# Performance work log

Measured on AMD Instinct MI355X. Metric: run time of the kernel, lower is better.

## Reference

```python
import jax, jax.numpy as jnp
import numpy as np

H = 128
NH = 8
HD = H // NH  # 16
TANH_ALPHA = 10.0
LN_EPS = 1e-5


def _layer_norm(x, g, b):
    mu = jnp.mean(x, axis=-1, keepdims=True)
    var = jnp.mean((x - mu) ** 2, axis=-1, keepdims=True)
    return (x - mu) / jnp.sqrt(var + LN_EPS) * g + b


def setup_inputs() -> dict:
    key = jax.random.key(0)
    ks = jax.random.split(key, 24)
    B, N = 1024, 500

    def p(k, shape):
        return jax.random.normal(k, shape, dtype=jnp.float32) * 0.05

    inp = {
        "node_embeddings": jax.random.normal(ks[0], (B, N, H), jnp.float32),
        "graph_embeddings": jax.random.normal(ks[1], (B, H), jnp.float32),
        "first_node": jax.random.randint(ks[2], (B,), 0, N, jnp.int32),
        "current_node": jax.random.randint(ks[3], (B,), 0, N, jnp.int32),
        "mask": jax.random.randint(ks[4], (B, N), 0, 2, jnp.int32),
        # linear_first: Linear(384, 128)
        "W_first": p(ks[5], (H, 3 * H)),
        "b_first": p(ks[6], (H,)),
        # ln1 / ln2
        "g1": jnp.ones((H,), jnp.float32),
        "beta1": jnp.zeros((H,), jnp.float32),
        "g2": jnp.ones((H,), jnp.float32),
        "beta2": jnp.zeros((H,), jnp.float32),
        # LSTM(128,128) single layer, gate order i,f,g,o
        "W_ih": p(ks[7], (4 * H, H)),
        "W_hh": p(ks[8], (4 * H, H)),
        "b_ih": p(ks[9], (4 * H,)),
        "b_hh": p(ks[10], (4 * H,)),
        # attention / output projections (no bias)
        "Wq": p(ks[11], (H, H)),
        "Wk": p(ks[12], (H, H)),
        "Wv": p(ks[13], (H, H)),
        "Wproj": p(ks[14], (H, H)),
        # logitk: Linear(128,128) with bias
        "Wlk": p(ks[15], (H, H)),
        "blk": p(ks[16], (H,)),
    }
    return inp


def reference(node_embeddings, graph_embeddings, W_first, b_first, g1, beta1,
              W_ih, W_hh, b_ih, b_hh, g2, beta2, Wq, Wk, Wv, Wproj, Wlk, blk,
              first_node, current_node, mask):
    B, N, _ = node_embeddings.shape
    dt = node_embeddings.dtype

    # build_cache: K/V/logitK projections of all node embeddings
    ck = node_embeddings @ Wk.T                # [B,N,128]
    cv = node_embeddings @ Wv.T                # [B,N,128]
    lk = node_embeddings @ Wlk.T + blk         # [B,N,128]

    # context construction
    bidx = jnp.arange(B)
    first_emb = node_embeddings[bidx, first_node]    # [B,128]
    cur_emb = node_embeddings[bidx, current_node]    # [B,128]
    context = jnp.concatenate([graph_embeddings, first_emb, cur_emb], axis=1)
    context = _layer_norm(context @ W_first.T + b_first, g1, beta1)

    # single LSTM step from zero state (build_cache resets h,c to 0)
    gates = context @ W_ih.T + b_ih + b_hh           # h_prev = 0 -> no W_hh term
    i, f, g, o = jnp.split(gates, 4, axis=-1)
    c = jax.nn.sigmoid(i) * jnp.tanh(g)              # c_prev = 0
    h = jax.nn.sigmoid(o) * jnp.tanh(c)
    ctx = _layer_norm(h, g2, beta2)

    # multi-head single-query attention; note (e h) split: head is the FAST dim
    q = (ctx @ Wq.T).reshape(B, HD, NH).transpose(0, 2, 1)       # [B,h,e]
    k = ck.reshape(B, N, HD, NH).transpose(0, 3, 1, 2)           # [B,h,N,e]
    v = cv.reshape(B, N, HD, NH).transpose(0, 3, 1, 2)           # [B,h,N,e]
    maskf = mask.astype(dt)
    scores = jnp.einsum('bhe,bhne->bhn', q, k) / np.sqrt(HD) + maskf[:, None, :]
    att = jax.nn.softmax(scores, axis=-1)
    oh = jnp.einsum('bhn,bhne->bhe', att, v)                     # [B,h,e]
    att_out = oh.reshape(B, H)                                   # (h e): h slow, e fast

    context_emb = att_out @ Wproj.T                              # [B,128]
    comp = jnp.einsum('be,bne->bn', lk, context_emb[:, None, :].squeeze(1)[:, :][None].squeeze(0) if False else context_emb) if False else jnp.einsum('bne,be->bn', lk, context_emb)
    comp = comp / np.sqrt(H)
    comp = TANH_ALPHA * jnp.tanh(comp)
    out = jnp.where(mask == 1, -jnp.inf, comp)
    return out
```

## Files before the change

kernel.cpp:

```cpp
#include <hip/hip_runtime.h>
#include <math.h>

#define NBATCH 1024
#define NNODE  500
#define HDIM   128
#define NHEAD  8
#define G1K    4
#define RSQRT_H 0.08838834764831845f
#define MASK_NEG (-1e30f)

__device__ __forceinline__ float wave_sum64(float v) {
    #pragma unroll
    for (int off = 32; off >= 1; off >>= 1) v += __shfl_xor(v, off, 64);
    return v;
}
__device__ __forceinline__ float wave_max64(float v) {
    #pragma unroll
    for (int off = 32; off >= 1; off >>= 1) v = fmaxf(v, __shfl_xor(v, off, 64));
    return v;
}

template<int G>
__device__ __forceinline__ void block_ln(float (&x)[G], const float* __restrict__ gw,
                                         const float* __restrict__ bw,
                                         int t, int lane, int wv, float (*wpart)[G])
{
    float s[G];
    #pragma unroll
    for (int g = 0; g < G; ++g) s[g] = x[g];
    #pragma unroll
    for (int off = 32; off >= 1; off >>= 1) {
        #pragma unroll
        for (int g = 0; g < G; ++g) s[g] += __shfl_xor(s[g], off, 64);
    }
    if (lane == 0) {
        #pragma unroll
        for (int g = 0; g < G; ++g) wpart[wv][g] = s[g];
    }
    __syncthreads();
    float mu[G];
    #pragma unroll
    for (int g = 0; g < G; ++g) mu[g] = (wpart[0][g] + wpart[1][g]) * (1.f/128.f);
    __syncthreads();
    #pragma unroll
    for (int g = 0; g < G; ++g) { float d = x[g] - mu[g]; s[g] = d * d; }
    #pragma unroll
    for (int off = 32; off >= 1; off >>= 1) {
        #pragma unroll
        for (int g = 0; g < G; ++g) s[g] += __shfl_xor(s[g], off, 64);
    }
    if (lane == 0) {
        #pragma unroll
        for (int g = 0; g < G; ++g) wpart[wv][g] = s[g];
    }
    __syncthreads();
    float gv = gw[t], bv = bw[t];
    #pragma unroll
    for (int g = 0; g < G; ++g) {
        float var = (wpart[0][g] + wpart[1][g]) * (1.f/128.f);
        x[g] = (x[g] - mu[g]) / sqrtf(var + 1e-5f) * gv + bv;
    }
    __syncthreads();
}

__global__ __launch_bounds__(128) void k1_context(
    const float* __restrict__ node, const float* __restrict__ graph,
    const int* __restrict__ firstn, const int* __restrict__ curn,
    const float* __restrict__ W_first, const float* __restrict__ b_first,
    const float* __restrict__ g1, const float* __restrict__ beta1,
    const float* __restrict__ W_ih, const float* __restrict__ b_ih,
    const float* __restrict__ b_hh, const float* __restrict__ g2,
    const float* __restrict__ beta2, const float* __restrict__ Wq,
    const float* __restrict__ Wk, float* __restrict__ qW_out)
{
    const int t = threadIdx.x;
    const int lane = t & 63, wv = t >> 6;
    const int b0 = blockIdx.x * G1K;
    __shared__ float ctx[G1K][384];
    __shared__ float bufB[G1K][128];
    __shared__ float wpart[2][G1K];

    #pragma unroll
    for (int g = 0; g < G1K; ++g) {
        int b = b0 + g;
        ctx[g][t]       = graph[b*HDIM + t];
        ctx[g][128 + t] = node[((size_t)b*NNODE + firstn[b])*HDIM + t];
        ctx[g][256 + t] = node[((size_t)b*NNODE + curn[b])*HDIM + t];
    }
    __syncthreads();

    float x[G1K];
    {
        float bf = b_first[t];
        #pragma unroll
        for (int g = 0; g < G1K; ++g) x[g] = bf;
        for (int j = 0; j < 384; ++j) {
            float w = W_first[t*384 + j];
            #pragma unroll
            for (int g = 0; g < G1K; ++g) x[g] += ctx[g][j] * w;
        }
    }
    block_ln<G1K>(x, g1, beta1, t, lane, wv, wpart);

    #pragma unroll
    for (int g = 0; g < G1K; ++g) bufB[g][t] = x[g];
    __syncthreads();

    float gi[G1K], gg[G1K], go[G1K];
    {
        float bi = b_ih[t]       + b_hh[t];
        float bg = b_ih[256 + t] + b_hh[256 + t];
        float bo = b_ih[384 + t] + b_hh[384 + t];
        #pragma unroll
        for (int g = 0; g < G1K; ++g) { gi[g] = bi; gg[g] = bg; go[g] = bo; }
        for (int j = 0; j < 128; ++j) {
            float wi = W_ih[(size_t)t*128 + j];
            float wg = W_ih[(size_t)(256 + t)*128 + j];
            float wo = W_ih[(size_t)(384 + t)*128 + j];
            #pragma unroll
            for (int g = 0; g < G1K; ++g) {
                float v = bufB[g][j];
                gi[g] += v * wi; gg[g] += v * wg; go[g] += v * wo;
            }
        }
    }
    #pragma unroll
    for (int g = 0; g < G1K; ++g) {
        float ig = 1.f / (1.f + expf(-gi[g]));
        float cc = ig * tanhf(gg[g]);
        float og = 1.f / (1.f + expf(-go[g]));
        x[g] = og * tanhf(cc);
    }
    block_ln<G1K>(x, g2, beta2, t, lane, wv, wpart);

    #pragma unroll
    for (int g = 0; g < G1K; ++g) bufB[g][t] = x[g];
    __syncthreads();

    float q8[G1K];
    #pragma unroll
    for (int g = 0; g < G1K; ++g) q8[g] = 0.f;
    for (int j = 0; j < 128; ++j) {
        float w = Wq[t*128 + j];
        #pragma unroll
        for (int g = 0; g < G1K; ++g) q8[g] += bufB[g][j] * w;
    }
    __syncthreads();
    #pragma unroll
    for (int g = 0; g < G1K; ++g) bufB[g][t] = q8[g];
    __syncthreads();

    for (int h = 0; h < NHEAD; ++h) {
        float a[G1K];
        #pragma unroll
        for (int g = 0; g < G1K; ++g) a[g] = 0.f;
        for (int e = 0; e < 16; ++e) {
            float w = Wk[(e*8 + h)*HDIM + t];
            #pragma unroll
            for (int g = 0; g < G1K; ++g) a[g] += bufB[g][e*8 + h] * w;
        }
        #pragma unroll
        for (int g = 0; g < G1K; ++g)
            qW_out[((size_t)(b0 + g)*NHEAD + h)*HDIM + t] = 0.25f * a[g];
    }
}

__global__ __launch_bounds__(256) void k2_flash(
    const float* __restrict__ node, const int* __restrict__ mask,
    const float* __restrict__ qW, const float* __restrict__ Wv,
    const float* __restrict__ Wproj, const float* __restrict__ Wlk,
    const float* __restrict__ blk, float* __restrict__ wce_out,
    float* __restrict__ bias_out)
{
    const int b = blockIdx.x;
    const int tid = threadIdx.x;
    const int lane = tid & 63;
    const int wave = tid >> 6;

    __shared__ float4 s_tile[64*32];
    __shared__ __align__(16) float s_qw[NHEAD*HDIM];
    __shared__ float  s_p[NHEAD*64];
    __shared__ float  s_m[NHEAD], s_l[NHEAD], s_c[NHEAD];
    __shared__ float  s_ao[HDIM], s_ce[HDIM];

    ((float4*)s_qw)[tid] = ((const float4*)(qW + (size_t)b*NHEAD*HDIM))[tid];
    if (tid < NHEAD) { s_m[tid] = -INFINITY; s_l[tid] = 0.f; }

    float4 acc[NHEAD];
    #pragma unroll
    for (int h = 0; h < NHEAD; ++h) acc[h] = make_float4(0.f, 0.f, 0.f, 0.f);

    const int sn = tid & 63;
    const int hp = tid >> 6;
    const int sg = tid >> 5;
    const int aq = tid & 31;

    const float* nodeb = node + (size_t)b*NNODE*HDIM;

    for (int tile = 0; tile < 8; ++tile) {
        const int base = tile*64;
        #pragma unroll
        for (int i = 0; i < 8; ++i) {
            int idx = i*256 + tid;
            int r = idx >> 5, qq = idx & 31;
            int gn = base + r;
            float4 v = make_float4(0.f, 0.f, 0.f, 0.f);
            if (gn < NNODE) v = *(const float4*)(nodeb + (size_t)gn*HDIM + qq*4);
            s_tile[r*32 + (qq ^ (r & 31))] = v;
        }
        __syncthreads();
        {
            float s0 = 0.f, s1 = 0.f;
            const int rb = sn*32, sw = sn & 31;
            const float4* qa = (const float4*)(s_qw + hp*HDIM);
            const float4* qb = (const float4*)(s_qw + (hp + 4)*HDIM);
            #pragma unroll 8
            for (int qq = 0; qq < 32; ++qq) {
                float4 nv = s_tile[rb + (qq ^ sw)];
                float4 av = qa[qq];
                float4 bv = qb[qq];
                s0 += nv.x*av.x + nv.y*av.y + nv.z*av.z + nv.w*av.w;
                s1 += nv.x*bv.x + nv.y*bv.y + nv.z*bv.z + nv.w*bv.w;
            }
            int gn = base + sn;
            if (gn < NNODE) {
                float mf = (float)mask[(size_t)b*NNODE + gn];
                s0 += mf; s1 += mf;
            } else { s0 = -INFINITY; s1 = -INFINITY; }
            s_p[hp*64 + sn] = s0;
            s_p[(hp + 4)*64 + sn] = s1;
        }
        __syncthreads();
        for (int hh = wave; hh < NHEAD; hh += 4) {
            float sv = s_p[hh*64 + lane];
            float mx = wave_max64(sv);
            float mO = s_m[hh];
            float mN = fmaxf(mO, mx);
            float pv = __expf(sv - mN);
            s_p[hh*64 + lane] = pv;
            float sm = wave_sum64(pv);
            if (lane == 0) {
                float corr = __expf(mO - mN);
                s_c[hh] = corr;
                s_l[hh] = s_l[hh]*corr + sm;
                s_m[hh] = mN;
            }
        }
        __syncthreads();
        {
            #pragma unroll
            for (int h = 0; h < NHEAD; ++h) {
                float c = s_c[h];
                acc[h].x *= c; acc[h].y *= c; acc[h].z *= c; acc[h].w *= c;
            }
            #pragma unroll
            for (int j = 0; j < 8; ++j) {
                int n = sg*8 + j;
                float4 nv = s_tile[n*32 + (aq ^ (n & 31))];
                #pragma unroll
                for (int h = 0; h < NHEAD; ++h) {
                    float p = s_p[h*64 + n];
                    acc[h].x += p*nv.x; acc[h].y += p*nv.y;
                    acc[h].z += p*nv.z; acc[h].w += p*nv.w;
                }
            }
        }
        __syncthreads();
    }
    #pragma unroll
    for (int h = 0; h < NHEAD; ++h) s_tile[(sg*8 + h)*32 + aq] = acc[h];
    __syncthreads();
    {
        const int h2 = tid >> 5, q2 = tid & 31;
        float4 tot = make_float4(0.f, 0.f, 0.f, 0.f);
        #pragma unroll
        for (int s = 0; s < 8; ++s) {
            float4 v = s_tile[(s*8 + h2)*32 + q2];
            tot.x += v.x; tot.y += v.y; tot.z += v.z; tot.w += v.w;
        }
        float inv = 1.f / s_l[h2];
        tot.x *= inv; tot.y *= inv; tot.z *= inv; tot.w *= inv;
        ((float4*)s_qw)[h2*32 + q2] = tot;
    }
    __syncthreads();
    if (tid < HDIM) {
        const int c = tid, h = c >> 4, e = c & 15;
        const int row = e*8 + h;
        float oh = 0.f;
        for (int d = 0; d < HDIM; ++d) oh += s_qw[h*HDIM + d] * Wv[row*HDIM + d];
        s_ao[c] = oh;
    }
    __syncthreads();
    if (tid < HDIM) {
        const int c = tid;
        float ce = 0.f;
        for (int j = 0; j < HDIM; ++j) ce += s_ao[j] * Wproj[c*HDIM + j];
        s_ce[c] = ce;
    }
    __syncthreads();
    if (tid < HDIM) {
        const int d = tid;
        float w = 0.f;
        for (int c = 0; c < HDIM; ++c) w += s_ce[c] * Wlk[c*HDIM + d];
        wce_out[(size_t)b*HDIM + d] = w * RSQRT_H;
        if (d == 0) {
            float bb = 0.f;
            for (int c = 0; c < HDIM; ++c) bb += s_ce[c] * blk[c];
            bias_out[b] = bb * RSQRT_H;
        }
    }
}

__global__ __launch_bounds__(256) void k3_out(
    const float* __restrict__ node, const int* __restrict__ mask,
    const float* __restrict__ wce, const float* __restrict__ biasv,
    float* __restrict__ out)
{
    const int slot = (int)((blockIdx.x*256u + threadIdx.x) >> 5);
    const int q = threadIdx.x & 31;
    const int b = slot / NNODE;
    const float4 nv = *(const float4*)(node + (size_t)slot*HDIM + q*4);
    const float4 wv = *(const float4*)(wce + (size_t)b*HDIM + q*4);
    float p = nv.x*wv.x + nv.y*wv.y + nv.z*wv.z + nv.w*wv.w;
    #pragma unroll
    for (int off = 16; off >= 1; off >>= 1) p += __shfl_xor(p, off, 32);
    if (q == 0) {
        float v = 10.f * tanhf(p + biasv[b]);
        out[slot] = (mask[slot] == 1) ? MASK_NEG : v;
    }
}

extern "C" void kernel_launch(void* const* d_in, const int* in_sizes, int n_in,
                              void* d_out, int out_size, void* d_ws, size_t ws_size,
                              hipStream_t stream) {
    const float* node    = (const float*)d_in[0];
    const float* graph   = (const float*)d_in[1];
    const int*   firstn  = (const int*)d_in[2];
    const int*   curn    = (const int*)d_in[3];
    const int*   mask    = (const int*)d_in[4];
    const float* W_first = (const float*)d_in[5];
    const float* b_first = (const float*)d_in[6];
    const float* g1      = (const float*)d_in[7];
    const float* beta1   = (const float*)d_in[8];
    const float* g2      = (const float*)d_in[9];
    const float* beta2   = (const float*)d_in[10];
    const float* W_ih    = (const float*)d_in[11];
    const float* b_ih    = (const float*)d_in[13];
    const float* b_hh    = (const float*)d_in[14];
    const float* Wq      = (const float*)d_in[15];
    const float* Wk      = (const float*)d_in[16];
    const float* Wv      = (const float*)d_in[17];
    const float* Wproj   = (const float*)d_in[18];
    const float* Wlk     = (const float*)d_in[19];
    const float* blk     = (const float*)d_in[20];
    float* out = (float*)d_out;

    float* qW    = (float*)d_ws;
    float* wce   = qW + (size_t)NBATCH*NHEAD*HDIM;
    float* biasv = wce + (size_t)NBATCH*HDIM;

    k1_context<<<NBATCH/G1K, 128, 0, stream>>>(node, graph, firstn, curn,
        W_first, b_first, g1, beta1, W_ih, b_ih, b_hh, g2, beta2, Wq, Wk, qW);
    k2_flash<<<NBATCH, 256, 0, stream>>>(node, mask, qW, Wv, Wproj, Wlk, blk,
        wce, biasv);
    k3_out<<<(NBATCH*NNODE)/8, 256, 0, stream>>>(node, mask, wce, biasv, out);
}
```

Before: 218.2 us.

## Split attention pass into per-chunk partial blocks plus a reduction kernel

After: 216.3 us. About the same (-0.9%).

```diff
diff --git a/kernel.cpp b/kernel.cpp
--- a/kernel.cpp
+++ b/kernel.cpp
@@ -6,6 +6,9 @@
 #define HDIM   128
 #define NHEAD  8
 #define G1K    4
+#define SPLIT  8
+#define CHUNK  64
+#define PSTRIDE 1056
 #define RSQRT_H 0.08838834764831845f
 #define MASK_NEG (-1e30f)
 
@@ -165,7 +168,173 @@
     }
 }
 
-__global__ __launch_bounds__(256) void k2_flash(
+__global__ __launch_bounds__(256) void k2a_partial(
+    const float* __restrict__ node, const int* __restrict__ mask,
+    const float* __restrict__ qW, float* __restrict__ part)
+{
+    const int b = blockIdx.x >> 3;
+    const int s = blockIdx.x & (SPLIT - 1);
+    const int tid = threadIdx.x;
+    const int lane = tid & 63;
+    const int wave = tid >> 6;
+    const int n0 = s * CHUNK;
+
+    __shared__ float4 s_tile[CHUNK*32];
+    __shared__ __align__(16) float s_qw[NHEAD*HDIM];
+    __shared__ float  s_p[NHEAD*CHUNK];
+
+    ((float4*)s_qw)[tid] = ((const float4*)(qW + (size_t)b*NHEAD*HDIM))[tid];
+
+    const float* nodeb = node + (size_t)b*NNODE*HDIM;
+    float* pbase = part + (size_t)blockIdx.x * PSTRIDE;
+
+    #pragma unroll
+    for (int i = 0; i < 8; ++i) {
+        int idx = i*256 + tid;
+        int r = idx >> 5, qq = idx & 31;
+        int gn = n0 + r;
+        float4 v = make_float4(0.f, 0.f, 0.f, 0.f);
+        if (gn < NNODE) v = *(const float4*)(nodeb + (size_t)gn*HDIM + qq*4);
+        s_tile[r*32 + (qq ^ (r & 31))] = v;
+    }
+    __syncthreads();
+
+    {
+        const int sn = tid & 63;
+        const int hp = tid >> 6;
+        float s0 = 0.f, s1 = 0.f;
+        const int rb = sn*32, sw = sn & 31;
+        const float4* qa = (const float4*)(s_qw + hp*HDIM);
+        const float4* qb = (const float4*)(s_qw + (hp + 4)*HDIM);
+        #pragma unroll 8
+        for (int qq = 0; qq < 32; ++qq) {
+            float4 nv = s_tile[rb + (qq ^ sw)];
+            float4 av = qa[qq];
+            float4 bv = qb[qq];
+            s0 += nv.x*av.x + nv.y*av.y + nv.z*av.z + nv.w*av.w;
+            s1 += nv.x*bv.x + nv.y*bv.y + nv.z*bv.z + nv.w*bv.w;
+        }
+        int gn = n0 + sn;
+        if (gn < NNODE) {
+            float mf = (float)mask[(size_t)b*NNODE + gn];
+            s0 += mf; s1 += mf;
+        } else { s0 = -INFINITY; s1 = -INFINITY; }
+        s_p[hp*64 + sn] = s0;
+        s_p[(hp + 4)*64 + sn] = s1;
+    }
+    __syncthreads();
+
+    for (int hh = wave; hh < NHEAD; hh += 4) {
+        float sv = s_p[hh*64 + lane];
+        float mx = wave_max64(sv);
+        float pv = (mx == -INFINITY) ? 0.f : __expf(sv - mx);
+        s_p[hh*64 + lane] = pv;
+        float sm = wave_sum64(pv);
+        if (lane == 0) {
+            pbase[hh]     = mx;
+            pbase[8 + hh] = sm;
+        }
+    }
+    __syncthreads();
+
+    const int sg = tid >> 5;
+    const int aq = tid & 31;
+    float4 acc[NHEAD];
+    #pragma unroll
+    for (int h = 0; h < NHEAD; ++h) acc[h] = make_float4(0.f, 0.f, 0.f, 0.f);
+    #pragma unroll
+    for (int j = 0; j < 8; ++j) {
+        int n = sg*8 + j;
+        float4 nv = s_tile[n*32 + (aq ^ (n & 31))];
+        #pragma unroll
+        for (int h = 0; h < NHEAD; ++h) {
+            float p = s_p[h*64 + n];
+            acc[h].x += p*nv.x; acc[h].y += p*nv.y;
+            acc[h].z += p*nv.z; acc[h].w += p*nv.w;
+        }
+    }
+    __syncthreads();
+    #pragma unroll
+    for (int h = 0; h < NHEAD; ++h) s_tile[(sg*8 + h)*32 + aq] = acc[h];
+    __syncthreads();
+    {
+        const int h2 = tid >> 5, q2 = tid & 31;
+        float4 tot = make_float4(0.f, 0.f, 0.f, 0.f);
+        #pragma unroll
+        for (int ss = 0; ss < 8; ++ss) {
+            float4 v = s_tile[(ss*8 + h2)*32 + q2];
+            tot.x += v.x; tot.y += v.y; tot.z += v.z; tot.w += v.w;
+        }
+        *(float4*)(pbase + 16 + h2*HDIM + q2*4) = tot;
+    }
+}
+
+__global__ __launch_bounds__(256) void k2b_reduce(
+    const float* __restrict__ part, const float* __restrict__ Wv,
+    const float* __restrict__ Wproj, const float* __restrict__ Wlk,
+    const float* __restrict__ blk, float* __restrict__ wce_out,
+    float* __restrict__ bias_out)
+{
+    const int b = blockIdx.x;
+    const int tid = threadIdx.x;
+    __shared__ __align__(16) float s_an[NHEAD*HDIM];
+    __shared__ float s_ao[HDIM], s_ce[HDIM];
+
+    {
+        const int h = tid >> 5, q = tid & 31;
+        const float* pb = part + (size_t)b*SPLIT*PSTRIDE;
+        float m[SPLIT], l[SPLIT];
+        float gm = -INFINITY;
+        #pragma unroll
+        for (int s = 0; s < SPLIT; ++s) {
+            m[s] = pb[s*PSTRIDE + h];
+            l[s] = pb[s*PSTRIDE + 8 + h];
+            gm = fmaxf(gm, m[s]);
+        }
+        float lsum = 0.f;
+        float4 tot = make_float4(0.f, 0.f, 0.f, 0.f);
+        #pragma unroll
+        for (int s = 0; s < SPLIT; ++s) {
+            float f = __expf(m[s] - gm);
+            lsum += l[s] * f;
+            float4 v = *(const float4*)(pb + s*PSTRIDE + 16 + h*HDIM + q*4);
+            tot.x += f*v.x; tot.y += f*v.y; tot.z += f*v.z; tot.w += f*v.w;
+        }
+        float inv = 1.f / lsum;
+        tot.x *= inv; tot.y *= inv; tot.z *= inv; tot.w *= inv;
+        *(float4*)(s_an + h*HDIM + q*4) = tot;
+    }
+    __syncthreads();
+
+    if (tid < HDIM) {
+        const int c = tid, h = c >> 4, e = c & 15;
+        const int row = e*8 + h;
+        float oh = 0.f;
+        for (int d = 0; d < HDIM; ++d) oh += s_an[h*HDIM + d] * Wv[row*HDIM + d];
+        s_ao[c] = oh;
+    }
+    __syncthreads();
+    if (tid < HDIM) {
+        const int c = tid;
+        float ce = 0.f;
+        for (int j = 0; j < HDIM; ++j) ce += s_ao[j] * Wproj[c*HDIM + j];
+        s_ce[c] = ce;
+    }
+    __syncthreads();
+    if (tid < HDIM) {
+        const int d = tid;
+        float w = 0.f;
+        for (int c = 0; c < HDIM; ++c) w += s_ce[c] * Wlk[c*HDIM + d];
+        wce_out[(size_t)b*HDIM + d] = w * RSQRT_H;
+        if (d == 0) {
+            float bb = 0.f;
+            for (int c = 0; c < HDIM; ++c) bb += s_ce[c] * blk[c];
+            bias_out[b] = bb * RSQRT_H;
+        }
+    }
+}
+
+__global__ __launch_bounds__(256) void k2_flash_mono(
     const float* __restrict__ node, const int* __restrict__ mask,
     const float* __restrict__ qW, const float* __restrict__ Wv,
     const float* __restrict__ Wproj, const float* __restrict__ Wlk,
@@ -194,7 +363,6 @@
     const int hp = tid >> 6;
     const int sg = tid >> 5;
     const int aq = tid & 31;
-
     const float* nodeb = node + (size_t)b*NNODE*HDIM;
 
     for (int tile = 0; tile < 8; ++tile) {
@@ -358,10 +526,19 @@
     float* qW    = (float*)d_ws;
     float* wce   = qW + (size_t)NBATCH*NHEAD*HDIM;
     float* biasv = wce + (size_t)NBATCH*HDIM;
+    float* part  = biasv + NBATCH;
+    const size_t need = ((size_t)NBATCH*NHEAD*HDIM + (size_t)NBATCH*HDIM + NBATCH
+                         + (size_t)NBATCH*SPLIT*PSTRIDE) * sizeof(float);
 
     k1_context<<<NBATCH/G1K, 128, 0, stream>>>(node, graph, firstn, curn,
         W_first, b_first, g1, beta1, W_ih, b_ih, b_hh, g2, beta2, Wq, Wk, qW);
-    k2_flash<<<NBATCH, 256, 0, stream>>>(node, mask, qW, Wv, Wproj, Wlk, blk,
-        wce, biasv);
+    if (ws_size >= need) {
+        k2a_partial<<<NBATCH*SPLIT, 256, 0, stream>>>(node, mask, qW, part);
+        k2b_reduce<<<NBATCH, 256, 0, stream>>>(part, Wv, Wproj, Wlk, blk,
+            wce, biasv);
+    } else {
+        k2_flash_mono<<<NBATCH, 256, 0, stream>>>(node, mask, qW, Wv, Wproj,
+            Wlk, blk, wce, biasv);
+    }
     k3_out<<<(NBATCH*NNODE)/8, 256, 0, stream>>>(node, mask, wce, biasv, out);
 }
```
